# Kernel tuning notes

Hardware: AMD Instinct MI355X
Metric: run time of the kernel (lower is better)

## Reference

```python
import jax, jax.numpy as jnp
import numpy as np

N, M = 8192, 8192
N_POS, N_NEG = 2_000_000, 8_000_000


def setup_inputs() -> dict:
    key = jax.random.key(0)
    k1, k2, k3, k4, k5, k6, k7 = jax.random.split(key, 7)
    return {
        "drug_protein_reconstruct": jax.random.normal(k1, (N, M), dtype=jnp.float32),
        "drug_protein": jax.random.uniform(k2, (N, M), dtype=jnp.float32),
        "alpha": jax.random.uniform(k3, (1,), dtype=jnp.float32),
        "pos_x_index": jax.random.randint(k4, (N_POS,), 0, N, dtype=jnp.int64 if jax.config.jax_enable_x64 else jnp.int32),
        "pos_y_index": jax.random.randint(k5, (N_POS,), 0, M, dtype=jnp.int64 if jax.config.jax_enable_x64 else jnp.int32),
        "neg_x_index": jax.random.randint(k6, (N_NEG,), 0, N, dtype=jnp.int64 if jax.config.jax_enable_x64 else jnp.int32),
        "neg_y_index": jax.random.randint(k7, (N_NEG,), 0, M, dtype=jnp.int64 if jax.config.jax_enable_x64 else jnp.int32),
    }


def reference(drug_protein_reconstruct, drug_protein, alpha,
              pos_x_index, pos_y_index, neg_x_index, neg_y_index):
    # Fused gather -> subtract -> square -> sum (equivalent to dense MSE matrix
    # followed by fancy indexing, but without materializing the full loss_mat).
    a = alpha[0]
    pos_diff = (drug_protein_reconstruct[pos_x_index, pos_y_index]
                - drug_protein[pos_x_index, pos_y_index])
    neg_diff = (drug_protein_reconstruct[neg_x_index, neg_y_index]
                - drug_protein[neg_x_index, neg_y_index])
    pos_sum = jnp.sum(pos_diff * pos_diff)
    neg_sum = jnp.sum(neg_diff * neg_diff)
    return pos_sum * ((1.0 - a) * 0.5) + neg_sum * (a * 0.5)
```

## Files before the change

### kernel.cpp

```cpp
#include <hip/hip_runtime.h>

#define BLOCK 256
#define GRID 2048

__global__ __launch_bounds__(BLOCK) void dti_pu_loss_kernel(
    const float* __restrict__ R,
    const float* __restrict__ D,
    const float* __restrict__ alpha,
    const int* __restrict__ px, const int* __restrict__ py, int npos,
    const int* __restrict__ nx, const int* __restrict__ ny, int nneg,
    float* __restrict__ out)
{
    const int tid    = blockIdx.x * BLOCK + threadIdx.x;
    const int stride = gridDim.x * BLOCK;

    float pos_acc = 0.0f;
    float neg_acc = 0.0f;

    {
        const int n4 = npos >> 2;
        const int4* px4 = (const int4*)px;
        const int4* py4 = (const int4*)py;
        for (int i = tid; i < n4; i += stride) {
            int4 xs = px4[i];
            int4 ys = py4[i];
            int o0 = (xs.x << 13) + ys.x;
            int o1 = (xs.y << 13) + ys.y;
            int o2 = (xs.z << 13) + ys.z;
            int o3 = (xs.w << 13) + ys.w;
            float d0 = R[o0] - D[o0];
            float d1 = R[o1] - D[o1];
            float d2 = R[o2] - D[o2];
            float d3 = R[o3] - D[o3];
            pos_acc += d0 * d0 + d1 * d1 + d2 * d2 + d3 * d3;
        }
        for (int i = (n4 << 2) + tid; i < npos; i += stride) {
            int o = (px[i] << 13) + py[i];
            float d = R[o] - D[o];
            pos_acc += d * d;
        }
    }

    {
        const int n4 = nneg >> 2;
        const int4* nx4 = (const int4*)nx;
        const int4* ny4 = (const int4*)ny;
        for (int i = tid; i < n4; i += stride) {
            int4 xs = nx4[i];
            int4 ys = ny4[i];
            int o0 = (xs.x << 13) + ys.x;
            int o1 = (xs.y << 13) + ys.y;
            int o2 = (xs.z << 13) + ys.z;
            int o3 = (xs.w << 13) + ys.w;
            float d0 = R[o0] - D[o0];
            float d1 = R[o1] - D[o1];
            float d2 = R[o2] - D[o2];
            float d3 = R[o3] - D[o3];
            neg_acc += d0 * d0 + d1 * d1 + d2 * d2 + d3 * d3;
        }
        for (int i = (n4 << 2) + tid; i < nneg; i += stride) {
            int o = (nx[i] << 13) + ny[i];
            float d = R[o] - D[o];
            neg_acc += d * d;
        }
    }

    const float a = alpha[0];
    float v = pos_acc * ((1.0f - a) * 0.5f) + neg_acc * (a * 0.5f);

    #pragma unroll
    for (int off = 32; off > 0; off >>= 1)
        v += __shfl_down(v, off, 64);

    __shared__ float sdata[BLOCK / 64];
    const int lane = threadIdx.x & 63;
    const int wave = threadIdx.x >> 6;
    if (lane == 0) sdata[wave] = v;
    __syncthreads();
    if (threadIdx.x == 0) {
        float s = 0.0f;
        #pragma unroll
        for (int w = 0; w < BLOCK / 64; ++w) s += sdata[w];
        atomicAdd(out, s);
    }
}

extern "C" void kernel_launch(void* const* d_in, const int* in_sizes, int n_in,
                              void* d_out, int out_size, void* d_ws, size_t ws_size,
                              hipStream_t stream) {
    const float* R     = (const float*)d_in[0];
    const float* D     = (const float*)d_in[1];
    const float* alpha = (const float*)d_in[2];
    const int*   px    = (const int*)d_in[3];
    const int*   py    = (const int*)d_in[4];
    const int*   nx    = (const int*)d_in[5];
    const int*   ny    = (const int*)d_in[6];
    const int    npos  = in_sizes[3];
    const int    nneg  = in_sizes[5];

    float* out = (float*)d_out;

    hipMemsetAsync(out, 0, sizeof(float), stream);

    dti_pu_loss_kernel<<<GRID, BLOCK, 0, stream>>>(
        R, D, alpha, px, py, npos, nx, ny, nneg, out);
}
```

Measured before the change: 826.2 us.

## Process gathers in row-band passes to keep working set cache-resident

Splits the gather into four passes, each handling only indices whose row falls in one 2048-row band of the matrices, so the random accesses of a pass touch a smaller region that may fit in the large last-level cache. The cost is that the index arrays (80 MB total) are reread four times and each pass adds a branch per element that diverges within a wave. Unroll is disabled on the inner loops, which reduces memory-level parallelism per thread.

```diff
diff --git a/kernel.cpp b/kernel.cpp
--- a/kernel.cpp
+++ b/kernel.cpp
@@ -2,6 +2,8 @@
 
 #define BLOCK 256
 #define GRID 2048
+#define LOG_RPB 11
+#define NB 4
 
 __global__ __launch_bounds__(BLOCK) void dti_pu_loss_kernel(
     const float* __restrict__ R,
@@ -12,57 +14,49 @@
     float* __restrict__ out)
 {
     const int tid    = blockIdx.x * BLOCK + threadIdx.x;
-    const int stride = gridDim.x * BLOCK;
+    const int stride = GRID * BLOCK;
 
     float pos_acc = 0.0f;
     float neg_acc = 0.0f;
 
-    {
-        const int n4 = npos >> 2;
-        const int4* px4 = (const int4*)px;
-        const int4* py4 = (const int4*)py;
-        for (int i = tid; i < n4; i += stride) {
+    const int np4 = npos >> 2;
+    const int nn4 = nneg >> 2;
+    const int4* __restrict__ px4 = (const int4*)px;
+    const int4* __restrict__ py4 = (const int4*)py;
+    const int4* __restrict__ nx4 = (const int4*)nx;
+    const int4* __restrict__ ny4 = (const int4*)ny;
+
+    #pragma unroll 1
+    for (int p = 0; p < NB; ++p) {
+        #pragma unroll 1
+        for (int i = tid; i < np4; i += stride) {
             int4 xs = px4[i];
             int4 ys = py4[i];
-            int o0 = (xs.x << 13) + ys.x;
-            int o1 = (xs.y << 13) + ys.y;
-            int o2 = (xs.z << 13) + ys.z;
-            int o3 = (xs.w << 13) + ys.w;
-            float d0 = R[o0] - D[o0];
-            float d1 = R[o1] - D[o1];
-            float d2 = R[o2] - D[o2];
-            float d3 = R[o3] - D[o3];
-            pos_acc += d0 * d0 + d1 * d1 + d2 * d2 + d3 * d3;
+            if ((xs.x >> LOG_RPB) == p) { int o = (xs.x << 13) + ys.x; float d = R[o] - D[o]; pos_acc += d * d; }
+            if ((xs.y >> LOG_RPB) == p) { int o = (xs.y << 13) + ys.y; float d = R[o] - D[o]; pos_acc += d * d; }
+            if ((xs.z >> LOG_RPB) == p) { int o = (xs.z << 13) + ys.z; float d = R[o] - D[o]; pos_acc += d * d; }
+            if ((xs.w >> LOG_RPB) == p) { int o = (xs.w << 13) + ys.w; float d = R[o] - D[o]; pos_acc += d * d; }
         }
-        for (int i = (n4 << 2) + tid; i < npos; i += stride) {
-            int o = (px[i] << 13) + py[i];
-            float d = R[o] - D[o];
-            pos_acc += d * d;
+        #pragma unroll 1
+        for (int i = tid; i < nn4; i += stride) {
+            int4 xs = nx4[i];
+            int4 ys = ny4[i];
+            if ((xs.x >> LOG_RPB) == p) { int o = (xs.x << 13) + ys.x; float d = R[o] - D[o]; neg_acc += d * d; }
+            if ((xs.y >> LOG_RPB) == p) { int o = (xs.y << 13) + ys.y; float d = R[o] - D[o]; neg_acc += d * d; }
+            if ((xs.z >> LOG_RPB) == p) { int o = (xs.z << 13) + ys.z; float d = R[o] - D[o]; neg_acc += d * d; }
+            if ((xs.w >> LOG_RPB) == p) { int o = (xs.w << 13) + ys.w; float d = R[o] - D[o]; neg_acc += d * d; }
         }
     }
 
-    {
-        const int n4 = nneg >> 2;
-        const int4* nx4 = (const int4*)nx;
-        const int4* ny4 = (const int4*)ny;
-        for (int i = tid; i < n4; i += stride) {
-            int4 xs = nx4[i];
-            int4 ys = ny4[i];
-            int o0 = (xs.x << 13) + ys.x;
-            int o1 = (xs.y << 13) + ys.y;
-            int o2 = (xs.z << 13) + ys.z;
-            int o3 = (xs.w << 13) + ys.w;
-            float d0 = R[o0] - D[o0];
-            float d1 = R[o1] - D[o1];
-            float d2 = R[o2] - D[o2];
-            float d3 = R[o3] - D[o3];
-            neg_acc += d0 * d0 + d1 * d1 + d2 * d2 + d3 * d3;
-        }
-        for (int i = (n4 << 2) + tid; i < nneg; i += stride) {
-            int o = (nx[i] << 13) + ny[i];
-            float d = R[o] - D[o];
-            neg_acc += d * d;
-        }
+    for (int i = (np4 << 2) + tid; i < npos; i += stride) {
+        int o = (px[i] << 13) + py[i];
+        float d = R[o] - D[o];
+        pos_acc += d * d;
+    }
+    for (int i = (nn4 << 2) + tid; i < nneg; i += stride) {
+        int o = (nx[i] << 13) + ny[i];
+        float d = R[o] - D[o];
+        neg_acc += d * d;
     }
 
     const float a = alpha[0];
```

Measured after the change: 821.6 us. About the same (-0.6%).
